# Performance work log

Hardware: AMD Instinct MI355X
Metric: run time of the kernel (lower is better)

## Reference

```python
import jax, jax.numpy as jnp
import numpy as np

EPS = 1e-8

def setup_inputs() -> dict:
    key = jax.random.key(0)
    k1, k2, k3, k4 = jax.random.split(key, 4)
    B, S, D = 64, 512, 512
    emb1 = jax.random.normal(k1, (B, S, D), dtype=jnp.float32)
    emb2 = jax.random.normal(k2, (B, S, D), dtype=jnp.float32)
    # contiguous prefix attention masks (first n tokens valid), as assumed by the original
    len1 = jax.random.randint(k3, (B,), S // 4, S + 1)
    len2 = jax.random.randint(k4, (B,), S // 4, S + 1)
    pos = jnp.arange(S)
    mask1 = (pos[None, :] < len1[:, None]).astype(jnp.int32)
    mask2 = (pos[None, :] < len2[:, None]).astype(jnp.int32)
    return {"article_1_emb": emb1, "article_2_emb": emb2,
            "article_1_att_mask": mask1, "article_2_att_mask": mask2}


def reference(article_1_emb, article_2_emb, article_1_att_mask, article_2_att_mask):
    # L2-normalize token embeddings (cosine similarity = dot of normalized vectors)
    def l2n(x):
        n = jnp.sqrt(jnp.sum(x * x, axis=-1, keepdims=True))
        return x / jnp.maximum(n, EPS)

    e1 = l2n(article_1_emb)   # [B, S1, D]
    e2 = l2n(article_2_emb)   # [B, S2, D]
    sim = jnp.einsum('bid,bjd->bij', e1, e2)  # [B, S1, S2] pairwise cosine sims

    m1 = article_1_att_mask.astype(jnp.bool_)  # [B, S1]
    m2 = article_2_att_mask.astype(jnp.bool_)  # [B, S2]
    NEG = jnp.float32(-1e9)

    # max over valid j for each valid i, and max over valid i for each valid j
    row_max = jnp.max(jnp.where(m2[:, None, :], sim, NEG), axis=2)  # [B, S1]
    col_max = jnp.max(jnp.where(m1[:, :, None], sim, NEG), axis=1)  # [B, S2]
    row_sum = jnp.sum(jnp.where(m1, row_max, 0.0), axis=1)          # [B]
    col_sum = jnp.sum(jnp.where(m2, col_max, 0.0), axis=1)          # [B]

    n1 = jnp.sum(article_1_att_mask, axis=1).astype(jnp.float32)
    n2 = jnp.sum(article_2_att_mask, axis=1).astype(jnp.float32)
    return (row_sum + col_sum) / (n1 + n2)
```

## Files before the change

### kernel.cpp

```cpp
#include <hip/hip_runtime.h>
#include <hip/hip_bf16.h>


typedef __attribute__((ext_vector_type(8))) short bf16x8;
typedef __attribute__((ext_vector_type(4))) float f32x4;

#define NEGBIG (-1e9f)
#define CAST_LDS(p) ((__attribute__((address_space(3))) void*)(p))
#define CAST_G(p)   ((const __attribute__((address_space(1))) void*)(p))

__device__ __forceinline__ unsigned packbf2_hw(float lo, float hi) {
    __hip_bfloat162 h = __float22bfloat162_rn(float2{lo, hi});
    union { __hip_bfloat162 h; unsigned u; } c; c.h = h;
    return c.u;
}

__global__ __launch_bounds__(256)
void prep_kernel(float* __restrict__ e1, float* __restrict__ e2,
                 float* __restrict__ inv1, float* __restrict__ inv2)
{
    const int lane = threadIdx.x & 63;
    const int w    = threadIdx.x >> 6;
    const int row  = blockIdx.x * 4 + w;
    const bool is1 = row < 32768;
    const int  r   = is1 ? row : row - 32768;
    float* src = (is1 ? e1 : e2) + (size_t)r * 512;

    const float4* s4 = reinterpret_cast<const float4*>(src);
    float4 a = s4[lane * 2];
    float4 c = s4[lane * 2 + 1];

    uint4 p;
    p.x = packbf2_hw(a.x, a.y);
    p.y = packbf2_hw(a.z, a.w);
    p.z = packbf2_hw(c.x, c.y);
    p.w = packbf2_hw(c.z, c.w);
    reinterpret_cast<uint4*>(src)[lane] = p;

    float ss = a.x*a.x + a.y*a.y + a.z*a.z + a.w*a.w
             + c.x*c.x + c.y*c.y + c.z*c.z + c.w*c.w;
    #pragma unroll
    for (int m = 32; m; m >>= 1) ss += __shfl_xor(ss, m);
    if (lane == 0) {
        float iv = 1.0f / fmaxf(sqrtf(ss), 1e-8f);
        (is1 ? inv1 : inv2)[r] = iv;
    }
}

__global__ __launch_bounds__(256, 4)
void sim_kernel(const ushort* __restrict__ n1, const ushort* __restrict__ n2,
                const int* __restrict__ m1g, const int* __restrict__ m2g,
                const float* __restrict__ inv1, const float* __restrict__ inv2,
                float* __restrict__ rowmax_p,
                float* __restrict__ colmax_p)
{
    const int rt  = blockIdx.x;
    const int ct  = blockIdx.y;
    const int b   = blockIdx.z;
    const int tid = threadIdx.x;
    const int lane = tid & 63;
    const int w    = tid >> 6;
    const int wm   = w >> 1;
    const int wn   = w & 1;
    const int q    = lane >> 4;
    const int ln   = lane & 15;
    const int nb   = ct * 128;

    __shared__ __align__(16) ushort sA[2][128 * 32];
    __shared__ __align__(16) ushort sB[2][128 * 32];
    __shared__ float spr[2][128];
    __shared__ float spc[2][128];
    __shared__ int   sm1[128], sm2[128];
    __shared__ float sinv1[128], sinv2[128];

    if (tid < 128) {
        sm1[tid]   = m1g[b * 512 + rt * 128 + tid];
        sinv1[tid] = inv1[b * 512 + rt * 128 + tid];
    } else {
        int t = tid - 128;
        sm2[t]   = m2g[b * 512 + nb + t];
        sinv2[t] = inv2[b * 512 + nb + t];
    }

    const int gc = (lane & 3) ^ ((lane >> 2) & 3) ^ ((lane >> 4) & 3);
    const int r0 = w * 16 + (lane >> 2);
    const ushort* gA0 = n1 + (size_t)(b * 512 + rt * 128 + r0) * 1024 + gc * 8;
    const ushort* gA1 = gA0 + (size_t)64 * 1024;
    const ushort* gB0 = n2 + (size_t)(b * 512 + nb + r0) * 1024 + gc * 8;
    const ushort* gB1 = gB0 + (size_t)64 * 1024;

    const int sln = (ln & 3) ^ ((ln >> 2) & 3);
    int aoff[4], boff[4];
    #pragma unroll
    for (int mt = 0; mt < 4; ++mt)
        aoff[mt] = (wm * 64 + mt * 16 + ln) * 32 + ((q ^ sln) << 3);
    #pragma unroll
    for (int nt = 0; nt < 4; ++nt)
        boff[nt] = (wn * 64 + nt * 16 + ln) * 32 + ((q ^ sln) << 3);

    f32x4 acc[4][4];
    #pragma unroll
    for (int i = 0; i < 4; ++i)
        #pragma unroll
        for (int j = 0; j < 4; ++j)
            acc[i][j] = (f32x4){0.f, 0.f, 0.f, 0.f};

    __builtin_amdgcn_global_load_lds(CAST_G(gA0), CAST_LDS(&sA[0][w * 512]), 16, 0, 0);
    __builtin_amdgcn_global_load_lds(CAST_G(gA1), CAST_LDS(&sA[0][2048 + w * 512]), 16, 0, 0);
    __builtin_amdgcn_global_load_lds(CAST_G(gB0), CAST_LDS(&sB[0][w * 512]), 16, 0, 0);
    __builtin_amdgcn_global_load_lds(CAST_G(gB1), CAST_LDS(&sB[0][2048 + w * 512]), 16, 0, 0);
    __syncthreads();

    #pragma unroll 2
    for (int k = 0; k < 16; ++k) {
        const int p = k & 1;
        if (k < 15) {
            const int k1 = (k + 1) * 32;
            __builtin_amdgcn_global_load_lds(CAST_G(gA0 + k1), CAST_LDS(&sA[p ^ 1][w * 512]), 16, 0, 0);
            __builtin_amdgcn_global_load_lds(CAST_G(gA1 + k1), CAST_LDS(&sA[p ^ 1][2048 + w * 512]), 16, 0, 0);
            __builtin_amdgcn_global_load_lds(CAST_G(gB0 + k1), CAST_LDS(&sB[p ^ 1][w * 512]), 16, 0, 0);
            __builtin_amdgcn_global_load_lds(CAST_G(gB1 + k1), CAST_LDS(&sB[p ^ 1][2048 + w * 512]), 16, 0, 0);
        }
        bf16x8 af[4], bfr[4];
        #pragma unroll
        for (int mt = 0; mt < 4; ++mt)
            af[mt] = *reinterpret_cast<const bf16x8*>(&sA[p][aoff[mt]]);
        #pragma unroll
        for (int nt = 0; nt < 4; ++nt)
            bfr[nt] = *reinterpret_cast<const bf16x8*>(&sB[p][boff[nt]]);
        #pragma unroll
        for (int mt = 0; mt < 4; ++mt)
            #pragma unroll
            for (int nt = 0; nt < 4; ++nt)
                acc[mt][nt] = __builtin_amdgcn_mfma_f32_16x16x32_bf16(
                    af[mt], bfr[nt], acc[mt][nt], 0, 0, 0);
        __syncthreads();
    }

    float invj[4];
    f32x4 invi[4];
    #pragma unroll
    for (int nt = 0; nt < 4; ++nt)
        invj[nt] = sinv2[wn * 64 + nt * 16 + ln];
    #pragma unroll
    for (int mt = 0; mt < 4; ++mt)
        #pragma unroll
        for (int rg = 0; rg < 4; ++rg)
            invi[mt][rg] = sinv1[wm * 64 + mt * 16 + q * 4 + rg];
    #pragma unroll
    for (int mt = 0; mt < 4; ++mt)
        #pragma unroll
        for (int nt = 0; nt < 4; ++nt)
            acc[mt][nt] = acc[mt][nt] * (invi[mt] * invj[nt]);

    #pragma unroll
    for (int mt = 0; mt < 4; ++mt) {
        #pragma unroll
        for (int rg = 0; rg < 4; ++rg) {
            float rm = NEGBIG;
            #pragma unroll
            for (int nt = 0; nt < 4; ++nt) {
                float s = sm2[wn * 64 + nt * 16 + ln] ? acc[mt][nt][rg] : NEGBIG;
                rm = fmaxf(rm, s);
            }
            rm = fmaxf(rm, __shfl_xor(rm, 1));
            rm = fmaxf(rm, __shfl_xor(rm, 2));
            rm = fmaxf(rm, __shfl_xor(rm, 4));
            rm = fmaxf(rm, __shfl_xor(rm, 8));
            if (ln == 0) spr[wn][wm * 64 + mt * 16 + q * 4 + rg] = rm;
        }
    }
    #pragma unroll
    for (int nt = 0; nt < 4; ++nt) {
        float cm = NEGBIG;
        #pragma unroll
        for (int mt = 0; mt < 4; ++mt)
            #pragma unroll
            for (int rg = 0; rg < 4; ++rg) {
                float s = sm1[wm * 64 + mt * 16 + q * 4 + rg] ? acc[mt][nt][rg] : NEGBIG;
                cm = fmaxf(cm, s);
            }
        cm = fmaxf(cm, __shfl_xor(cm, 16));
        cm = fmaxf(cm, __shfl_xor(cm, 32));
        if (lane < 16) spc[wm][wn * 64 + nt * 16 + ln] = cm;
    }
    __syncthreads();
    if (tid < 128) {
        rowmax_p[((size_t)b * 4 + ct) * 512 + rt * 128 + tid] =
            fmaxf(spr[0][tid], spr[1][tid]);
        colmax_p[((size_t)b * 4 + rt) * 512 + nb + tid] =
            fmaxf(spc[0][tid], spc[1][tid]);
    }
}

__global__ __launch_bounds__(256)
void final_kernel(const int* __restrict__ m1g, const int* __restrict__ m2g,
                  const float* __restrict__ rowmax_p, const float* __restrict__ colmax_p,
                  float* __restrict__ out)
{
    const int b = blockIdx.x;
    const int tid = threadIdx.x;
    const int lane = tid & 63;
    const int w = tid >> 6;

    float sum = 0.f;
    float nn  = 0.f;
    for (int j = tid; j < 512; j += 256) {
        int mm1 = m1g[b * 512 + j];
        int mm2 = m2g[b * 512 + j];
        nn += (float)(mm1 + mm2);
        const float* rp = rowmax_p + (size_t)b * 2048 + j;
        float rm = fmaxf(fmaxf(rp[0], rp[512]), fmaxf(rp[1024], rp[1536]));
        if (mm1) sum += rm;
        const float* cp = colmax_p + (size_t)b * 2048 + j;
        float cm = fmaxf(fmaxf(cp[0], cp[512]), fmaxf(cp[1024], cp[1536]));
        if (mm2) sum += cm;
    }
    #pragma unroll
    for (int m = 32; m; m >>= 1) {
        sum += __shfl_xor(sum, m);
        nn  += __shfl_xor(nn, m);
    }
    __shared__ float ssum[4], snn[4];
    if (lane == 0) { ssum[w] = sum; snn[w] = nn; }
    __syncthreads();
    if (tid == 0) {
        float S = ssum[0] + ssum[1] + ssum[2] + ssum[3];
        float N = snn[0] + snn[1] + snn[2] + snn[3];
        out[b] = S / N;
    }
}

extern "C" void kernel_launch(void* const* d_in, const int* in_sizes, int n_in,
                              void* d_out, int out_size, void* d_ws, size_t ws_size,
                              hipStream_t stream) {
    float* e1 = (float*)d_in[0];
    float* e2 = (float*)d_in[1];
    const int* m1 = (const int*)d_in[2];
    const int* m2 = (const int*)d_in[3];
    float* out = (float*)d_out;

    float* ws = (float*)d_ws;
    float* inv1     = ws;
    float* inv2     = ws + 32768;
    float* rowmax_p = ws + 65536;
    float* colmax_p = ws + 196608;

    prep_kernel<<<16384, 256, 0, stream>>>(e1, e2, inv1, inv2);
    sim_kernel<<<dim3(4, 4, 64), 256, 0, stream>>>((const ushort*)e1, (const ushort*)e2,
                                                   m1, m2, inv1, inv2,
                                                   rowmax_p, colmax_p);
    final_kernel<<<64, 256, 0, stream>>>(m1, m2, rowmax_p, colmax_p, out);
}
```

Baseline: 194.0 us.

## Fuse bf16 conversion and norm computation into the similarity GEMM kernel

Removes the separate prep pass, which overwrote the fp32 inputs with bf16 and wrote inverse norms to workspace. The similarity kernel now reads fp32 tiles straight into registers, accumulates sums of squares, converts to bf16 and stores into swizzled LDS, with a register-level prefetch two k-steps ahead. Inverse norms are reduced at the end of the kernel and then applied. This drops a full read/write pass over the inputs and one launch. In exchange, each tile's fp32 data is re-read from global memory or cache by four blocks, register pressure rises, and the async global-to-LDS loads are replaced by ordinary loads plus LDS stores.

```diff
diff --git a/kernel.cpp b/kernel.cpp
--- a/kernel.cpp
+++ b/kernel.cpp
@@ -6,8 +6,6 @@
 typedef __attribute__((ext_vector_type(4))) float f32x4;
 
 #define NEGBIG (-1e9f)
-#define CAST_LDS(p) ((__attribute__((address_space(3))) void*)(p))
-#define CAST_G(p)   ((const __attribute__((address_space(1))) void*)(p))
 
 __device__ __forceinline__ unsigned packbf2_hw(float lo, float hi) {
     __hip_bfloat162 h = __float22bfloat162_rn(float2{lo, hi});
@@ -16,43 +14,10 @@
 }
 
 __global__ __launch_bounds__(256)
-void prep_kernel(float* __restrict__ e1, float* __restrict__ e2,
-                 float* __restrict__ inv1, float* __restrict__ inv2)
-{
-    const int lane = threadIdx.x & 63;
-    const int w    = threadIdx.x >> 6;
-    const int row  = blockIdx.x * 4 + w;
-    const bool is1 = row < 32768;
-    const int  r   = is1 ? row : row - 32768;
-    float* src = (is1 ? e1 : e2) + (size_t)r * 512;
-
-    const float4* s4 = reinterpret_cast<const float4*>(src);
-    float4 a = s4[lane * 2];
-    float4 c = s4[lane * 2 + 1];
-
-    uint4 p;
-    p.x = packbf2_hw(a.x, a.y);
-    p.y = packbf2_hw(a.z, a.w);
-    p.z = packbf2_hw(c.x, c.y);
-    p.w = packbf2_hw(c.z, c.w);
-    reinterpret_cast<uint4*>(src)[lane] = p;
-
-    float ss = a.x*a.x + a.y*a.y + a.z*a.z + a.w*a.w
-             + c.x*c.x + c.y*c.y + c.z*c.z + c.w*c.w;
-    #pragma unroll
-    for (int m = 32; m; m >>= 1) ss += __shfl_xor(ss, m);
-    if (lane == 0) {
-        float iv = 1.0f / fmaxf(sqrtf(ss), 1e-8f);
-        (is1 ? inv1 : inv2)[r] = iv;
-    }
-}
-
-__global__ __launch_bounds__(256, 4)
-void sim_kernel(const ushort* __restrict__ n1, const ushort* __restrict__ n2,
-                const int* __restrict__ m1g, const int* __restrict__ m2g,
-                const float* __restrict__ inv1, const float* __restrict__ inv2,
-                float* __restrict__ rowmax_p,
-                float* __restrict__ colmax_p)
+void sim_fused(const float* __restrict__ e1, const float* __restrict__ e2,
+               const int* __restrict__ m1g, const int* __restrict__ m2g,
+               float* __restrict__ rowmax_p,
+               float* __restrict__ colmax_p)
 {
     const int rt  = blockIdx.x;
     const int ct  = blockIdx.y;
@@ -73,21 +38,16 @@
     __shared__ int   sm1[128], sm2[128];
     __shared__ float sinv1[128], sinv2[128];
 
-    if (tid < 128) {
-        sm1[tid]   = m1g[b * 512 + rt * 128 + tid];
-        sinv1[tid] = inv1[b * 512 + rt * 128 + tid];
-    } else {
-        int t = tid - 128;
-        sm2[t]   = m2g[b * 512 + nb + t];
-        sinv2[t] = inv2[b * 512 + nb + t];
-    }
-
-    const int gc = (lane & 3) ^ ((lane >> 2) & 3) ^ ((lane >> 4) & 3);
-    const int r0 = w * 16 + (lane >> 2);
-    const ushort* gA0 = n1 + (size_t)(b * 512 + rt * 128 + r0) * 1024 + gc * 8;
-    const ushort* gA1 = gA0 + (size_t)64 * 1024;
-    const ushort* gB0 = n2 + (size_t)(b * 512 + nb + r0) * 1024 + gc * 8;
-    const ushort* gB1 = gB0 + (size_t)64 * 1024;
+    if (tid < 128) sm1[tid] = m1g[b * 512 + rt * 128 + tid];
+    else           sm2[tid - 128] = m2g[b * 512 + nb + (tid - 128)];
+
+    const int r = tid >> 1;
+    const int h = tid & 1;
+    const int s = (r ^ (r >> 2)) & 3;
+    const float* gA = e1 + ((size_t)(b * 512 + rt * 128 + r)) * 512 + h * 16;
+    const float* gB = e2 + ((size_t)(b * 512 + nb + r)) * 512 + h * 16;
+    const int wo0 = r * 32 + (((2 * h)     ^ s) << 3);
+    const int wo1 = r * 32 + (((2 * h + 1) ^ s) << 3);
 
     const int sln = (ln & 3) ^ ((ln >> 2) & 3);
     int aoff[4], boff[4];
@@ -98,6 +58,38 @@
     for (int nt = 0; nt < 4; ++nt)
         boff[nt] = (wn * 64 + nt * 16 + ln) * 32 + ((q ^ sln) << 3);
 
+    float ssA = 0.f, ssB = 0.f;
+    float4 ra[4], rb[4];
+
+    auto LOADK = [&](int kf) {
+        const float4* pa = reinterpret_cast<const float4*>(gA + kf);
+        const float4* pb = reinterpret_cast<const float4*>(gB + kf);
+        ra[0] = pa[0]; ra[1] = pa[1]; ra[2] = pa[2]; ra[3] = pa[3];
+        rb[0] = pb[0]; rb[1] = pb[1]; rb[2] = pb[2]; rb[3] = pb[3];
+    };
+    auto CVTWRITE = [&](int p) {
+        #pragma unroll
+        for (int i = 0; i < 4; ++i) {
+            ssA += ra[i].x * ra[i].x + ra[i].y * ra[i].y
+                 + ra[i].z * ra[i].z + ra[i].w * ra[i].w;
+            ssB += rb[i].x * rb[i].x + rb[i].y * rb[i].y
+                 + rb[i].z * rb[i].z + rb[i].w * rb[i].w;
+        }
+        uint4 u;
+        u.x = packbf2_hw(ra[0].x, ra[0].y); u.y = packbf2_hw(ra[0].z, ra[0].w);
+        u.z = packbf2_hw(ra[1].x, ra[1].y); u.w = packbf2_hw(ra[1].z, ra[1].w);
+        *reinterpret_cast<uint4*>(&sA[p][wo0]) = u;
+        u.x = packbf2_hw(ra[2].x, ra[2].y); u.y = packbf2_hw(ra[2].z, ra[2].w);
+        u.z = packbf2_hw(ra[3].x, ra[3].y); u.w = packbf2_hw(ra[3].z, ra[3].w);
+        *reinterpret_cast<uint4*>(&sA[p][wo1]) = u;
+        u.x = packbf2_hw(rb[0].x, rb[0].y); u.y = packbf2_hw(rb[0].z, rb[0].w);
+        u.z = packbf2_hw(rb[1].x, rb[1].y); u.w = packbf2_hw(rb[1].z, rb[1].w);
+        *reinterpret_cast<uint4*>(&sB[p][wo0]) = u;
+        u.x = packbf2_hw(rb[2].x, rb[2].y); u.y = packbf2_hw(rb[2].z, rb[2].w);
+        u.z = packbf2_hw(rb[3].x, rb[3].y); u.w = packbf2_hw(rb[3].z, rb[3].w);
+        *reinterpret_cast<uint4*>(&sB[p][wo1]) = u;
+    };
+
     f32x4 acc[4][4];
     #pragma unroll
     for (int i = 0; i < 4; ++i)
@@ -105,22 +97,14 @@
         for (int j = 0; j < 4; ++j)
             acc[i][j] = (f32x4){0.f, 0.f, 0.f, 0.f};
 
-    __builtin_amdgcn_global_load_lds(CAST_G(gA0), CAST_LDS(&sA[0][w * 512]), 16, 0, 0);
-    __builtin_amdgcn_global_load_lds(CAST_G(gA1), CAST_LDS(&sA[0][2048 + w * 512]), 16, 0, 0);
-    __builtin_amdgcn_global_load_lds(CAST_G(gB0), CAST_LDS(&sB[0][w * 512]), 16, 0, 0);
-    __builtin_amdgcn_global_load_lds(CAST_G(gB1), CAST_LDS(&sB[0][2048 + w * 512]), 16, 0, 0);
+    LOADK(0);
+    CVTWRITE(0);
+    LOADK(32);
     __syncthreads();
 
     #pragma unroll 2
     for (int k = 0; k < 16; ++k) {
         const int p = k & 1;
-        if (k < 15) {
-            const int k1 = (k + 1) * 32;
-            __builtin_amdgcn_global_load_lds(CAST_G(gA0 + k1), CAST_LDS(&sA[p ^ 1][w * 512]), 16, 0, 0);
-            __builtin_amdgcn_global_load_lds(CAST_G(gA1 + k1), CAST_LDS(&sA[p ^ 1][2048 + w * 512]), 16, 0, 0);
-            __builtin_amdgcn_global_load_lds(CAST_G(gB0 + k1), CAST_LDS(&sB[p ^ 1][w * 512]), 16, 0, 0);
-            __builtin_amdgcn_global_load_lds(CAST_G(gB1 + k1), CAST_LDS(&sB[p ^ 1][2048 + w * 512]), 16, 0, 0);
-        }
         bf16x8 af[4], bfr[4];
         #pragma unroll
         for (int mt = 0; mt < 4; ++mt)
@@ -128,6 +112,8 @@
         #pragma unroll
         for (int nt = 0; nt < 4; ++nt)
             bfr[nt] = *reinterpret_cast<const bf16x8*>(&sB[p][boff[nt]]);
+        if (k < 15) CVTWRITE(p ^ 1);
+        if (k < 14) LOADK((k + 2) * 32);
         #pragma unroll
         for (int mt = 0; mt < 4; ++mt)
             #pragma unroll
@@ -137,6 +123,14 @@
         __syncthreads();
     }
 
+    ssA += __shfl_xor(ssA, 1);
+    ssB += __shfl_xor(ssB, 1);
+    if (h == 0) {
+        sinv1[r] = 1.0f / fmaxf(sqrtf(ssA), 1e-8f);
+        sinv2[r] = 1.0f / fmaxf(sqrtf(ssB), 1e-8f);
+    }
+    __syncthreads();
+
     float invj[4];
     f32x4 invi[4];
     #pragma unroll
@@ -160,8 +154,8 @@
             float rm = NEGBIG;
             #pragma unroll
             for (int nt = 0; nt < 4; ++nt) {
-                float s = sm2[wn * 64 + nt * 16 + ln] ? acc[mt][nt][rg] : NEGBIG;
-                rm = fmaxf(rm, s);
+                float v = sm2[wn * 64 + nt * 16 + ln] ? acc[mt][nt][rg] : NEGBIG;
+                rm = fmaxf(rm, v);
             }
             rm = fmaxf(rm, __shfl_xor(rm, 1));
             rm = fmaxf(rm, __shfl_xor(rm, 2));
@@ -177,8 +171,8 @@
         for (int mt = 0; mt < 4; ++mt)
             #pragma unroll
             for (int rg = 0; rg < 4; ++rg) {
-                float s = sm1[wm * 64 + mt * 16 + q * 4 + rg] ? acc[mt][nt][rg] : NEGBIG;
-                cm = fmaxf(cm, s);
+                float v = sm1[wm * 64 + mt * 16 + q * 4 + rg] ? acc[mt][nt][rg] : NEGBIG;
+                cm = fmaxf(cm, v);
             }
         cm = fmaxf(cm, __shfl_xor(cm, 16));
         cm = fmaxf(cm, __shfl_xor(cm, 32));
@@ -234,21 +228,17 @@
 extern "C" void kernel_launch(void* const* d_in, const int* in_sizes, int n_in,
                               void* d_out, int out_size, void* d_ws, size_t ws_size,
                               hipStream_t stream) {
-    float* e1 = (float*)d_in[0];
-    float* e2 = (float*)d_in[1];
-    const int* m1 = (const int*)d_in[2];
-    const int* m2 = (const int*)d_in[3];
+    const float* e1 = (const float*)d_in[0];
+    const float* e2 = (const float*)d_in[1];
+    const int*   m1 = (const int*)d_in[2];
+    const int*   m2 = (const int*)d_in[3];
     float* out = (float*)d_out;
 
     float* ws = (float*)d_ws;
-    float* inv1     = ws;
-    float* inv2     = ws + 32768;
-    float* rowmax_p = ws + 65536;
-    float* colmax_p = ws + 196608;
-
-    prep_kernel<<<16384, 256, 0, stream>>>(e1, e2, inv1, inv2);
-    sim_kernel<<<dim3(4, 4, 64), 256, 0, stream>>>((const ushort*)e1, (const ushort*)e2,
-                                                   m1, m2, inv1, inv2,
-                                                   rowmax_p, colmax_p);
+    float* rowmax_p = ws;
+    float* colmax_p = ws + 131072;
+
+    sim_fused<<<dim3(4, 4, 64), 256, 0, stream>>>(e1, e2, m1, m2,
+                                                  rowmax_p, colmax_p);
     final_kernel<<<64, 256, 0, stream>>>(m1, m2, rowmax_p, colmax_p, out);
 }
```

New measurement: 183.8 us. -5.3%, faster.
